# Kernel tuning notes

Measured on AMD Instinct MI355X. Metric: run time of the kernel, lower is better.

## Reference

```python
import jax, jax.numpy as jnp
import numpy as np

OUT_FEATURES = 4096
IN_FEATURES = 4096
GROUP_SIZE = 16


def setup_inputs() -> dict:
    key = jax.random.key(0)
    k1, k2, k3, k4 = jax.random.split(key, 4)
    n_groups = OUT_FEATURES * IN_FEATURES // GROUP_SIZE
    x = jax.random.normal(k1, (8, 2048, IN_FEATURES), dtype=jnp.float32)
    weight_q = jax.random.randint(k2, (n_groups, GROUP_SIZE), 0, 16, dtype=jnp.int32).astype(jnp.int8)
    weight_norm = jax.random.uniform(k3, (n_groups, 1), dtype=jnp.float32).astype(jnp.float16)
    bias = jax.random.normal(k4, (OUT_FEATURES,), dtype=jnp.float32)
    return {"x": x, "weight_q": weight_q, "weight_norm": weight_norm, "bias": bias}


def reference(x, weight_q, weight_norm, bias):
    # block dequant: (q/15) * per-group scale, then reshape to [out, in]
    w = (weight_q.astype(jnp.float32) / 15.0) * weight_norm.astype(jnp.float32)
    w = w.reshape(OUT_FEATURES, IN_FEATURES)
    # F.linear: x @ w^T + bias
    return jnp.einsum('bsi,oi->bso', x, w) + bias
```

## Files before the change

### kernel.cpp

```cpp
#include <hip/hip_runtime.h>

#define MDIM 16384
#define NDIM 4096
#define KDIM 4096
#define BK   64
#define NT   (KDIM / BK)

typedef unsigned short u16;
typedef unsigned int   u32;
typedef __attribute__((ext_vector_type(8))) short bh8;
typedef __attribute__((ext_vector_type(4))) float f32x4;
typedef __attribute__((ext_vector_type(4))) int   i32x4;

__device__ __forceinline__ u16 f2bf(float f) {
  u32 u = __builtin_bit_cast(u32, f);
  u = (u + 0x7fffu + ((u >> 16) & 1u)) >> 16;
  return (u16)u;
}

__device__ __forceinline__ void gld16(const void* g, const void* lds) {
  __builtin_amdgcn_global_load_lds((const __attribute__((address_space(1))) u32*)g,
                                   (__attribute__((address_space(3))) u32*)lds, 16, 0, 0);
}

__global__ void cvt_x(const float* __restrict__ x, u16* __restrict__ xb) {
  size_t i = ((size_t)blockIdx.x * 256 + threadIdx.x) * 8;
  f32x4 a = *(const f32x4*)(x + i);
  f32x4 b = *(const f32x4*)(x + i + 4);
  bh8 o;
  o[0] = (short)f2bf(a[0]); o[1] = (short)f2bf(a[1]);
  o[2] = (short)f2bf(a[2]); o[3] = (short)f2bf(a[3]);
  o[4] = (short)f2bf(b[0]); o[5] = (short)f2bf(b[1]);
  o[6] = (short)f2bf(b[2]); o[7] = (short)f2bf(b[3]);
  *(bh8*)(xb + i) = o;
}

__global__ void deq_w(const int* __restrict__ qi, const void* __restrict__ nrm,
                      u16* __restrict__ wb) {
  __shared__ int s_q8, s_n32;
  if (threadIdx.x == 0) {
    int packed = 0;
    for (int t = 0; t < 64; ++t) {
      unsigned v = (unsigned)qi[t];
      if (v > 15u) packed = 1;
    }
    int n32 = 0;
    const u16* h = (const u16*)nrm;
    for (int t = 0; t < 64; ++t) {
      u16 b = h[t];
      if (b < 0x8000u && b > 0x3C00u) n32 = 1;
    }
    s_q8 = packed; s_n32 = n32;
  }
  __syncthreads();
  const bool q8 = (s_q8 != 0), n32 = (s_n32 != 0);

  int g = blockIdx.x * 256 + threadIdx.x;
  float s;
  if (n32) s = ((const float*)nrm)[g] * (1.0f / 15.0f);
  else {
    u16 hb = ((const u16*)nrm)[g];
    s = (float)__builtin_bit_cast(_Float16, hb) * (1.0f / 15.0f);
  }

  float q[16];
  if (q8) {
    i32x4 v = *(const i32x4*)((const unsigned char*)qi + (size_t)g * 16);
#pragma unroll
    for (int k = 0; k < 4; ++k) {
      int word = v[k];
      q[k * 4 + 0] = (float)(word & 255);
      q[k * 4 + 1] = (float)((word >> 8) & 255);
      q[k * 4 + 2] = (float)((word >> 16) & 255);
      q[k * 4 + 3] = (float)((word >> 24) & 255);
    }
  } else {
    const i32x4* p = (const i32x4*)(qi + (size_t)g * 16);
#pragma unroll
    for (int k = 0; k < 4; ++k) {
      i32x4 v = p[k];
      q[k * 4 + 0] = (float)v[0]; q[k * 4 + 1] = (float)v[1];
      q[k * 4 + 2] = (float)v[2]; q[k * 4 + 3] = (float)v[3];
    }
  }
  bh8 o0, o1;
#pragma unroll
  for (int j = 0; j < 8; ++j) o0[j] = (short)f2bf(q[j] * s);
#pragma unroll
  for (int j = 0; j < 8; ++j) o1[j] = (short)f2bf(q[8 + j] * s);
  *(bh8*)(wb + (size_t)g * 16) = o0;
  *(bh8*)(wb + (size_t)g * 16 + 8) = o1;
}

template <bool PRE>
__global__ __launch_bounds__(512, 2) void gemm_k(const void* __restrict__ Asrc,
                                                 const u16* __restrict__ Wbf,
                                                 const float* __restrict__ bias,
                                                 float* __restrict__ out) {
  __shared__ u16 lds[65536];
  const int tid = threadIdx.x;
  const int w = tid >> 6, l = tid & 63;
  const int wm = w >> 2, wn = w & 3;

  int bid = blockIdx.x;
  int wg = (bid & 7) * 128 + (bid >> 3);
  const int bm = wg >> 4;
  const int bn = wg & 15;

  const u16*   Abf  = (const u16*)Asrc;
  const float* Af32 = (const float*)Asrc;

  int srcOffA[4], srcOffB[4], srcOffA32[4], dstSwzA[4];
#pragma unroll
  for (int j = 0; j < 4; ++j) {
    int ci = (w * 4 + j) * 64 + l;
    int r = ci >> 3, c = ci & 7;
    int cs = c ^ (r & 7);
    srcOffB[j] = (bn * 256 + r) * 4096 + cs * 8;
    if (PRE) {
      srcOffA[j] = (bm * 256 + r) * 4096 + cs * 8;
    } else {
      srcOffA32[j] = (bm * 256 + r) * 4096 + c * 8;
      dstSwzA[j]   = r * 64 + cs * 8;
    }
  }

  const int ar = wm * 128 + (l & 15);
  const int br = wn * 64 + (l & 15);
  const int swz0 = (((l >> 4) + 0) ^ (l & 7)) * 8;
  const int swz1 = (((l >> 4) + 4) ^ (l & 7)) * 8;
  const int aoff0 = ar * 64 + swz0, aoff1 = ar * 64 + swz1;
  const int boff0 = 32768 + br * 64 + swz0, boff1 = 32768 + br * 64 + swz1;

  f32x4 acc[8][4];
#pragma unroll
  for (int mi = 0; mi < 8; ++mi)
#pragma unroll
    for (int ni = 0; ni < 4; ++ni) acc[mi][ni] = (f32x4){0.f, 0.f, 0.f, 0.f};

  auto STAGE = [&](int bufb, int kt) {
    const int kof = kt * 64;
#pragma unroll
    for (int j = 0; j < 4; ++j) {
      gld16(Wbf + srcOffB[j] + kof, &lds[32768 + bufb * 16384 + (w * 4 + j) * 512]);
      if (PRE) {
        gld16(Abf + srcOffA[j] + kof, &lds[bufb * 16384 + (w * 4 + j) * 512]);
      } else {
        const float* p = Af32 + srcOffA32[j] + kof;
        f32x4 v0 = *(const f32x4*)p;
        f32x4 v1 = *(const f32x4*)(p + 4);
        bh8 o;
        o[0] = (short)f2bf(v0[0]); o[1] = (short)f2bf(v0[1]);
        o[2] = (short)f2bf(v0[2]); o[3] = (short)f2bf(v0[3]);
        o[4] = (short)f2bf(v1[0]); o[5] = (short)f2bf(v1[1]);
        o[6] = (short)f2bf(v1[2]); o[7] = (short)f2bf(v1[3]);
        *(bh8*)&lds[bufb * 16384 + dstSwzA[j]] = o;
      }
    }
  };

  auto COMPUTE = [&](int bufb) {
    const int ab = bufb * 16384;
#pragma unroll
    for (int kk = 0; kk < 2; ++kk) {
      const int ao = ab + (kk ? aoff1 : aoff0);
      const int bo = ab + (kk ? boff1 : boff0);
      bh8 af[8], bfr[4];
#pragma unroll
      for (int mi = 0; mi < 8; ++mi) af[mi] = *(const bh8*)&lds[ao + mi * 1024];
#pragma unroll
      for (int ni = 0; ni < 4; ++ni) bfr[ni] = *(const bh8*)&lds[bo + ni * 1024];
#pragma unroll
      for (int mi = 0; mi < 8; ++mi)
#pragma unroll
        for (int ni = 0; ni < 4; ++ni)
          acc[mi][ni] = __builtin_amdgcn_mfma_f32_16x16x32_bf16(af[mi], bfr[ni],
                                                                acc[mi][ni], 0, 0, 0);
    }
  };

  int buf = 0;
  STAGE(0, 0);
  __syncthreads();
  for (int kt = 0; kt < NT - 1; ++kt) {
    STAGE(buf ^ 1, kt + 1);
    COMPUTE(buf);
    __syncthreads();
    buf ^= 1;
  }
  COMPUTE(buf);

  const int col0 = bn * 256 + wn * 64 + (l & 15);
  const int row0 = bm * 256 + wm * 128 + (l >> 4) * 4;
#pragma unroll
  for (int ni = 0; ni < 4; ++ni) {
    float bv = bias[col0 + ni * 16];
#pragma unroll
    for (int mi = 0; mi < 8; ++mi) {
      size_t base = (size_t)(row0 + mi * 16) * 4096 + (size_t)(col0 + ni * 16);
#pragma unroll
      for (int rr = 0; rr < 4; ++rr)
        out[base + (size_t)rr * 4096] = acc[mi][ni][rr] + bv;
    }
  }
}

extern "C" void kernel_launch(void* const* d_in, const int* in_sizes, int n_in,
                              void* d_out, int out_size, void* d_ws, size_t ws_size,
                              hipStream_t stream) {
  const float* x    = (const float*)d_in[0];
  const int*   wq   = (const int*)d_in[1];
  const void*  wn   = d_in[2];
  const float* bias = (const float*)d_in[3];
  float*       out  = (float*)d_out;

  const size_t needA = (size_t)MDIM * KDIM * 2;
  const size_t needW = (size_t)NDIM * KDIM * 2;

  if (ws_size >= needA + needW) {
    u16* xbf = (u16*)d_ws;
    u16* wbf = (u16*)((char*)d_ws + needA);
    cvt_x<<<dim3(32768), dim3(256), 0, stream>>>(x, xbf);
    deq_w<<<dim3(4096), dim3(256), 0, stream>>>(wq, wn, wbf);
    gemm_k<true><<<dim3(1024), dim3(512), 0, stream>>>(xbf, wbf, bias, out);
  } else if (ws_size >= needW) {
    u16* wbf = (u16*)d_ws;
    deq_w<<<dim3(4096), dim3(256), 0, stream>>>(wq, wn, wbf);
    gemm_k<false><<<dim3(1024), dim3(512), 0, stream>>>(x, wbf, bias, out);
  }
}
```

Baseline: 592.5 us.

## Rewrite bf16 GEMM main loop as 8-phase ping-pong schedule with split half-tile loads

Replaces the simple double-buffered GEMM loop with an eight-phase schedule. Each K-tile is split into half-tiles for A and B, global-to-LDS loads for future half-tiles are interleaved between MFMA phases, and explicit barriers, waitcnts and sched_barriers control ordering. MFMA sections are raised in priority with s_setprio so compute overlaps memory traffic more tightly and barrier stalls shrink. The change adds hand-managed vmcnt counting and more barriers, which is fragile and could stall or race if the counts are off.

```diff
diff --git a/kernel.cpp b/kernel.cpp
--- a/kernel.cpp
+++ b/kernel.cpp
@@ -3,8 +3,7 @@
 #define MDIM 16384
 #define NDIM 4096
 #define KDIM 4096
-#define BK   64
-#define NT   (KDIM / BK)
+#define NT   64
 
 typedef unsigned short u16;
 typedef unsigned int   u32;
@@ -40,16 +39,10 @@
   __shared__ int s_q8, s_n32;
   if (threadIdx.x == 0) {
     int packed = 0;
-    for (int t = 0; t < 64; ++t) {
-      unsigned v = (unsigned)qi[t];
-      if (v > 15u) packed = 1;
-    }
+    for (int t = 0; t < 64; ++t) { unsigned v = (unsigned)qi[t]; if (v > 15u) packed = 1; }
     int n32 = 0;
     const u16* h = (const u16*)nrm;
-    for (int t = 0; t < 64; ++t) {
-      u16 b = h[t];
-      if (b < 0x8000u && b > 0x3C00u) n32 = 1;
-    }
+    for (int t = 0; t < 64; ++t) { u16 b = h[t]; if (b < 0x8000u && b > 0x3C00u) n32 = 1; }
     s_q8 = packed; s_n32 = n32;
   }
   __syncthreads();
@@ -62,25 +55,22 @@
     u16 hb = ((const u16*)nrm)[g];
     s = (float)__builtin_bit_cast(_Float16, hb) * (1.0f / 15.0f);
   }
-
   float q[16];
   if (q8) {
     i32x4 v = *(const i32x4*)((const unsigned char*)qi + (size_t)g * 16);
 #pragma unroll
     for (int k = 0; k < 4; ++k) {
       int word = v[k];
-      q[k * 4 + 0] = (float)(word & 255);
-      q[k * 4 + 1] = (float)((word >> 8) & 255);
-      q[k * 4 + 2] = (float)((word >> 16) & 255);
-      q[k * 4 + 3] = (float)((word >> 24) & 255);
+      q[k*4+0] = (float)(word & 255);        q[k*4+1] = (float)((word >> 8) & 255);
+      q[k*4+2] = (float)((word >> 16) & 255); q[k*4+3] = (float)((word >> 24) & 255);
     }
   } else {
     const i32x4* p = (const i32x4*)(qi + (size_t)g * 16);
 #pragma unroll
     for (int k = 0; k < 4; ++k) {
       i32x4 v = p[k];
-      q[k * 4 + 0] = (float)v[0]; q[k * 4 + 1] = (float)v[1];
-      q[k * 4 + 2] = (float)v[2]; q[k * 4 + 3] = (float)v[3];
+      q[k*4+0] = (float)v[0]; q[k*4+1] = (float)v[1];
+      q[k*4+2] = (float)v[2]; q[k*4+3] = (float)v[3];
     }
   }
   bh8 o0, o1;
@@ -92,11 +82,10 @@
   *(bh8*)(wb + (size_t)g * 16 + 8) = o1;
 }
 
-template <bool PRE>
-__global__ __launch_bounds__(512, 2) void gemm_k(const void* __restrict__ Asrc,
-                                                 const u16* __restrict__ Wbf,
-                                                 const float* __restrict__ bias,
-                                                 float* __restrict__ out) {
+__global__ __launch_bounds__(512, 2) void gemm8(const u16* __restrict__ A,
+                                                const u16* __restrict__ B,
+                                                const float* __restrict__ bias,
+                                                float* __restrict__ out) {
   __shared__ u16 lds[65536];
   const int tid = threadIdx.x;
   const int w = tid >> 6, l = tid & 63;
@@ -107,24 +96,134 @@
   const int bm = wg >> 4;
   const int bn = wg & 15;
 
-  const u16*   Abf  = (const u16*)Asrc;
-  const float* Af32 = (const float*)Asrc;
-
-  int srcOffA[4], srcOffB[4], srcOffA32[4], dstSwzA[4];
+  const int cs8  = ((l & 7) ^ (l >> 3)) * 8;
+  const u16* aSrc = A + (size_t)(bm * 256 + w * 32 + (l >> 3)) * 4096 + cs8;
+  const u16* bSrc = B + (size_t)(bn * 256 + w * 32 + (l >> 3)) * 4096 + cs8;
+
+  const int fr  = (l & 15) * 64;
+  const int sz0 = (((l >> 4)) ^ (l & 7)) * 8;
+  const int sz1 = ((4 + (l >> 4)) ^ (l & 7)) * 8;
+
+  f32x4 acc[8][4];
+#pragma unroll
+  for (int mi = 0; mi < 8; ++mi)
+#pragma unroll
+    for (int ni = 0; ni < 4; ++ni) acc[mi][ni] = (f32x4){0.f, 0.f, 0.f, 0.f};
+
+  bh8 af[4][2], b0f[2][2], b1f[2][2];
+
+  auto STG = [&](int op, int h, int kt) {
+    const u16* s = (op ? bSrc : aSrc) + h * 65536 + kt * 64;
+    int d = (op ? 32768 : 0) + ((kt & 1) * 2 + h) * 8192 + w * 1024;
+    gld16(s,         &lds[d]);
+    gld16(s + 32768, &lds[d + 512]);
+  };
+  auto RDA = [&](int buf, int mp) {
+#pragma unroll
+    for (int q = 0; q < 4; ++q) {
+      int base = (buf * 2 + mp) * 8192 + (wm * 4 + q) * 1024 + fr;
+      af[q][0] = *(const bh8*)&lds[base + sz0];
+      af[q][1] = *(const bh8*)&lds[base + sz1];
+    }
+  };
+  auto RDB = [&](int buf, int np, bh8 (&bb)[2][2]) {
+#pragma unroll
+    for (int q = 0; q < 2; ++q) {
+      int base = 32768 + (buf * 2 + np) * 8192 + (wn * 2 + q) * 1024 + fr;
+      bb[q][0] = *(const bh8*)&lds[base + sz0];
+      bb[q][1] = *(const bh8*)&lds[base + sz1];
+    }
+  };
+  auto MM = [&](int mp, int np, bh8 (&bb)[2][2]) {
+    __builtin_amdgcn_s_setprio(1);
+#pragma unroll
+    for (int q = 0; q < 4; ++q)
+#pragma unroll
+      for (int r = 0; r < 2; ++r)
+#pragma unroll
+        for (int kk = 0; kk < 2; ++kk)
+          acc[q*2+mp][r*2+np] = __builtin_amdgcn_mfma_f32_16x16x32_bf16(
+              af[q][kk], bb[r][kk], acc[q*2+mp][r*2+np], 0, 0, 0);
+    __builtin_amdgcn_s_setprio(0);
+  };
+
+#define PH(BUF, MP, NP, BB, RA, RB, PRE) \
+  do { \
+    if (RA) RDA(BUF, MP); \
+    if (RB) RDB(BUF, NP, BB); \
+    PRE \
+    __builtin_amdgcn_s_barrier(); \
+    asm volatile("s_waitcnt lgkmcnt(0)"); \
+    __builtin_amdgcn_sched_barrier(0); \
+    MM(MP, NP, BB); \
+    __builtin_amdgcn_s_barrier(); \
+  } while (0)
+
+  STG(0, 0, 0); STG(1, 0, 0);
+  STG(0, 1, 0); STG(1, 1, 0);
+  STG(0, 0, 1); STG(1, 0, 1);
+  asm volatile("s_waitcnt vmcnt(4)");
+  __builtin_amdgcn_s_barrier();
+
+#pragma unroll 1
+  for (int i = 0; i < NT / 2 - 1; ++i) {
+    const int t1 = 2 * i + 1, t2 = 2 * i + 2, t3 = 2 * i + 3;
+    PH(0, 0, 0, b0f, 1, 1, { STG(0, 1, t1); });
+    PH(0, 0, 1, b1f, 0, 1, { STG(1, 1, t1); });
+    PH(0, 1, 0, b0f, 1, 0, { STG(0, 0, t2); });
+    PH(0, 1, 1, b1f, 0, 0, { STG(1, 0, t2); asm volatile("s_waitcnt vmcnt(4)"); });
+    PH(1, 0, 0, b0f, 1, 1, { STG(0, 1, t2); });
+    PH(1, 0, 1, b1f, 0, 1, { STG(1, 1, t2); });
+    PH(1, 1, 0, b0f, 1, 0, { STG(0, 0, t3); });
+    PH(1, 1, 1, b1f, 0, 0, { STG(1, 0, t3); asm volatile("s_waitcnt vmcnt(4)"); });
+  }
+  PH(0, 0, 0, b0f, 1, 1, { STG(0, 1, 63); });
+  PH(0, 0, 1, b1f, 0, 1, { STG(1, 1, 63); });
+  PH(0, 1, 0, b0f, 1, 0, {});
+  PH(0, 1, 1, b1f, 0, 0, { asm volatile("s_waitcnt vmcnt(0)"); });
+  PH(1, 0, 0, b0f, 1, 1, {});
+  PH(1, 0, 1, b1f, 0, 1, {});
+  PH(1, 1, 0, b0f, 1, 0, {});
+  PH(1, 1, 1, b1f, 0, 0, {});
+#undef PH
+
+  const int col0 = bn * 256 + wn * 64 + (l & 15);
+  const int row0 = bm * 256 + wm * 128 + (l >> 4) * 4;
+#pragma unroll
+  for (int ni = 0; ni < 4; ++ni) {
+    float bv = bias[col0 + ni * 16];
+#pragma unroll
+    for (int mi = 0; mi < 8; ++mi) {
+      size_t base = (size_t)(row0 + mi * 16) * 4096 + (size_t)(col0 + ni * 16);
+#pragma unroll
+      for (int rr = 0; rr < 4; ++rr)
+        out[base + (size_t)rr * 4096] = acc[mi][ni][rr] + bv;
+    }
+  }
+}
+
+__global__ __launch_bounds__(512, 2) void gemm_fb(const float* __restrict__ Af32,
+                                                  const u16* __restrict__ Wbf,
+                                                  const float* __restrict__ bias,
+                                                  float* __restrict__ out) {
+  __shared__ u16 lds[65536];
+  const int tid = threadIdx.x;
+  const int w = tid >> 6, l = tid & 63;
+  const int wm = w >> 2, wn = w & 3;
+  int bid = blockIdx.x;
+  int wg = (bid & 7) * 128 + (bid >> 3);
+  const int bm = wg >> 4, bn = wg & 15;
+
+  int srcOffB[4], srcOffA32[4], dstSwzA[4];
 #pragma unroll
   for (int j = 0; j < 4; ++j) {
     int ci = (w * 4 + j) * 64 + l;
     int r = ci >> 3, c = ci & 7;
     int cs = c ^ (r & 7);
-    srcOffB[j] = (bn * 256 + r) * 4096 + cs * 8;
-    if (PRE) {
-      srcOffA[j] = (bm * 256 + r) * 4096 + cs * 8;
-    } else {
-      srcOffA32[j] = (bm * 256 + r) * 4096 + c * 8;
-      dstSwzA[j]   = r * 64 + cs * 8;
-    }
-  }
-
+    srcOffB[j]   = (bn * 256 + r) * 4096 + cs * 8;
+    srcOffA32[j] = (bm * 256 + r) * 4096 + c * 8;
+    dstSwzA[j]   = r * 64 + cs * 8;
+  }
   const int ar = wm * 128 + (l & 15);
   const int br = wn * 64 + (l & 15);
   const int swz0 = (((l >> 4) + 0) ^ (l & 7)) * 8;
@@ -143,38 +242,33 @@
 #pragma unroll
     for (int j = 0; j < 4; ++j) {
       gld16(Wbf + srcOffB[j] + kof, &lds[32768 + bufb * 16384 + (w * 4 + j) * 512]);
-      if (PRE) {
-        gld16(Abf + srcOffA[j] + kof, &lds[bufb * 16384 + (w * 4 + j) * 512]);
-      } else {
-        const float* p = Af32 + srcOffA32[j] + kof;
-        f32x4 v0 = *(const f32x4*)p;
-        f32x4 v1 = *(const f32x4*)(p + 4);
-        bh8 o;
-        o[0] = (short)f2bf(v0[0]); o[1] = (short)f2bf(v0[1]);
-        o[2] = (short)f2bf(v0[2]); o[3] = (short)f2bf(v0[3]);
-        o[4] = (short)f2bf(v1[0]); o[5] = (short)f2bf(v1[1]);
-        o[6] = (short)f2bf(v1[2]); o[7] = (short)f2bf(v1[3]);
-        *(bh8*)&lds[bufb * 16384 + dstSwzA[j]] = o;
-      }
-    }
-  };
-
+      const float* p = Af32 + srcOffA32[j] + kof;
+      f32x4 v0 = *(const f32x4*)p;
+      f32x4 v1 = *(const f32x4*)(p + 4);
+      bh8 o;
+      o[0] = (short)f2bf(v0[0]); o[1] = (short)f2bf(v0[1]);
+      o[2] = (short)f2bf(v0[2]); o[3] = (short)f2bf(v0[3]);
+      o[4] = (short)f2bf(v1[0]); o[5] = (short)f2bf(v1[1]);
+      o[6] = (short)f2bf(v1[2]); o[7] = (short)f2bf(v1[3]);
+      *(bh8*)&lds[bufb * 16384 + dstSwzA[j]] = o;
+    }
+  };
   auto COMPUTE = [&](int bufb) {
     const int ab = bufb * 16384;
 #pragma unroll
     for (int kk = 0; kk < 2; ++kk) {
       const int ao = ab + (kk ? aoff1 : aoff0);
       const int bo = ab + (kk ? boff1 : boff0);
-      bh8 af[8], bfr[4];
-#pragma unroll
-      for (int mi = 0; mi < 8; ++mi) af[mi] = *(const bh8*)&lds[ao + mi * 1024];
+      bh8 afr[8], bfr[4];
+#pragma unroll
+      for (int mi = 0; mi < 8; ++mi) afr[mi] = *(const bh8*)&lds[ao + mi * 1024];
 #pragma unroll
       for (int ni = 0; ni < 4; ++ni) bfr[ni] = *(const bh8*)&lds[bo + ni * 1024];
 #pragma unroll
       for (int mi = 0; mi < 8; ++mi)
 #pragma unroll
         for (int ni = 0; ni < 4; ++ni)
-          acc[mi][ni] = __builtin_amdgcn_mfma_f32_16x16x32_bf16(af[mi], bfr[ni],
+          acc[mi][ni] = __builtin_amdgcn_mfma_f32_16x16x32_bf16(afr[mi], bfr[ni],
                                                                 acc[mi][ni], 0, 0, 0);
     }
   };
@@ -222,10 +316,10 @@
     u16* wbf = (u16*)((char*)d_ws + needA);
     cvt_x<<<dim3(32768), dim3(256), 0, stream>>>(x, xbf);
     deq_w<<<dim3(4096), dim3(256), 0, stream>>>(wq, wn, wbf);
-    gemm_k<true><<<dim3(1024), dim3(512), 0, stream>>>(xbf, wbf, bias, out);
+    gemm8<<<dim3(1024), dim3(512), 0, stream>>>(xbf, wbf, bias, out);
   } else if (ws_size >= needW) {
     u16* wbf = (u16*)d_ws;
     deq_w<<<dim3(4096), dim3(256), 0, stream>>>(wq, wn, wbf);
-    gemm_k<false><<<dim3(1024), dim3(512), 0, stream>>>(x, wbf, bias, out);
-  }
-}
+    gemm_fb<<<dim3(1024), dim3(512), 0, stream>>>(x, wbf, bias, out);
+  }
+}
```

After: 545.1 us. 8.0% less time.
